# Kernel tuning notes

Hardware: AMD Instinct MI355X
Metric: run time of the kernel (lower is better)

## Reference

```python
import jax, jax.numpy as jnp
import numpy as np

D_MODEL = 1024
N_HEADS = 16
D_K = D_MODEL // N_HEADS
D_FF = 4096
EPS = 1e-6


def setup_inputs() -> dict:
    key = jax.random.key(0)
    ks = jax.random.split(key, 8)
    s = 0.02
    return {
        "x": jax.random.normal(ks[0], (2, 2048, D_MODEL), dtype=jnp.float32),
        "Wq": jax.random.normal(ks[1], (D_MODEL, D_MODEL), dtype=jnp.float32) * s,
        "bq": jnp.zeros((D_MODEL,), jnp.float32),
        "Wk": jax.random.normal(ks[2], (D_MODEL, D_MODEL), dtype=jnp.float32) * s,
        "bk": jnp.zeros((D_MODEL,), jnp.float32),
        "Wv": jax.random.normal(ks[3], (D_MODEL, D_MODEL), dtype=jnp.float32) * s,
        "bv": jnp.zeros((D_MODEL,), jnp.float32),
        "Wo": jax.random.normal(ks[4], (D_MODEL, D_MODEL), dtype=jnp.float32) * s,
        "bo": jnp.zeros((D_MODEL,), jnp.float32),
        "W1": jax.random.normal(ks[5], (D_FF, D_MODEL), dtype=jnp.float32) * s,
        "b1": jnp.zeros((D_FF,), jnp.float32),
        "W2": jax.random.normal(ks[6], (D_MODEL, D_FF), dtype=jnp.float32) * s,
        "b2": jnp.zeros((D_MODEL,), jnp.float32),
        "g1": jnp.ones((D_MODEL,), jnp.float32),
        "be1": jnp.zeros((D_MODEL,), jnp.float32),
        "g2": jnp.ones((D_MODEL,), jnp.float32),
        "be2": jnp.zeros((D_MODEL,), jnp.float32),
    }


def _layernorm(x, gamma, beta):
    mean = x.mean(axis=-1, keepdims=True)
    var = ((x - mean) ** 2).mean(axis=-1, keepdims=True)
    return gamma * (x - mean) / jnp.sqrt(var + EPS) + beta


def _linear(x, W, b):
    # torch nn.Linear: y = x @ W.T + b
    return x @ W.T + b


def reference(x, Wq, bq, Wk, bk, Wv, bv, Wo, bo, W1, b1, W2, b2, g1, be1, g2, be2):
    B, S, _ = x.shape
    h = _layernorm(x, g1, be1)
    # project and split heads -> [B, H, S, d_k]
    Q = _linear(h, Wq, bq).reshape(B, S, N_HEADS, D_K).transpose(0, 2, 1, 3)
    K = _linear(h, Wk, bk).reshape(B, S, N_HEADS, D_K).transpose(0, 2, 1, 3)
    V = _linear(h, Wv, bv).reshape(B, S, N_HEADS, D_K).transpose(0, 2, 1, 3)
    scores = jnp.einsum("bhqd,bhkd->bhqk", Q, K) / jnp.sqrt(jnp.float32(D_K))
    attn = jax.nn.softmax(scores, axis=-1)
    ctx = jnp.einsum("bhqk,bhkd->bhqd", attn, V)
    ctx = ctx.transpose(0, 2, 1, 3).reshape(B, S, D_MODEL)
    x = x + _linear(ctx, Wo, bo)
    h2 = _layernorm(x, g2, be2)
    ff = _linear(jax.nn.gelu(_linear(h2, W1, b1), approximate=False), W2, b2)
    return x + ff
```

## Files before the change

### kernel.cpp

```cpp
#include <hip/hip_runtime.h>
#include <stdint.h>

#define D_MODEL 1024
#define N_HEADS 16
#define DKH     64
#define D_FF    4096
#define BATCH   2
#define SEQ     2048
#define M_TOK   (BATCH*SEQ)

typedef unsigned short u16;
typedef __attribute__((ext_vector_type(8))) short short8;
typedef __attribute__((ext_vector_type(4))) float f32x4;

__device__ __forceinline__ u16 f2b(float f){
  union { float f; uint32_t i; } c; c.f = f;
  uint32_t x = c.i;
  uint32_t r = x + 0x7fffu + ((x >> 16) & 1u);
  return (u16)(r >> 16);
}

__device__ __forceinline__ uint32_t pk_bf16(float a, float b){
  uint32_t d;
  asm("v_cvt_pk_bf16_f32 %0, %1, %2" : "=v"(d) : "v"(a), "v"(b));
  return d;
}

__device__ __forceinline__ void gl_lds16(const u16* g, u16* l){
  __builtin_amdgcn_global_load_lds(
      (const __attribute__((address_space(1))) void*)g,
      (__attribute__((address_space(3))) void*)l, 16, 0, 0);
}

#define MFMA16(a,b,c) __builtin_amdgcn_mfma_f32_16x16x32_bf16((a),(b),(c),0,0,0)

__global__ __launch_bounds__(256) void cvt_ln_kernel(
    const float* __restrict__ s0, const float* __restrict__ s1,
    const float* __restrict__ s2, const float* __restrict__ s3,
    const float* __restrict__ s4, const float* __restrict__ s5,
    u16* __restrict__ d0, u16* __restrict__ d1, u16* __restrict__ d2,
    u16* __restrict__ d3, u16* __restrict__ d4, u16* __restrict__ d5,
    const float* __restrict__ X, const float* __restrict__ G,
    const float* __restrict__ Bt, u16* __restrict__ O)
{
  __shared__ float psum[4], psum2[4];
  if (blockIdx.y == 6){
    const int row = blockIdx.x;
    const int t = threadIdx.x;
    float4 xv = *(const float4*)&X[(size_t)row * D_MODEL + t * 4];
    float s  = xv.x + xv.y + xv.z + xv.w;
    float s2 = xv.x*xv.x + xv.y*xv.y + xv.z*xv.z + xv.w*xv.w;
    #pragma unroll
    for (int off = 32; off >= 1; off >>= 1){
      s  += __shfl_down(s,  off, 64);
      s2 += __shfl_down(s2, off, 64);
    }
    const int wv = t >> 6, ln = t & 63;
    if (ln == 0){ psum[wv] = s; psum2[wv] = s2; }
    __syncthreads();
    float ts  = psum[0] + psum[1] + psum[2] + psum[3];
    float ts2 = psum2[0] + psum2[1] + psum2[2] + psum2[3];
    float mean = ts * (1.f / D_MODEL);
    float var  = ts2 * (1.f / D_MODEL) - mean * mean;
    float rstd = rsqrtf(var + 1e-6f);
    float4 g4 = *(const float4*)&G[t * 4];
    float4 b4 = *(const float4*)&Bt[t * 4];
    ushort4 o;
    o.x = f2b(g4.x * (xv.x - mean) * rstd + b4.x);
    o.y = f2b(g4.y * (xv.y - mean) * rstd + b4.y);
    o.z = f2b(g4.z * (xv.z - mean) * rstd + b4.z);
    o.w = f2b(g4.w * (xv.w - mean) * rstd + b4.w);
    *(ushort4*)&O[(size_t)row * D_MODEL + t * 4] = o;
    return;
  }
  const float* s; u16* d; int n;
  switch (blockIdx.y){
    case 0: s=s0; d=d0; n=D_MODEL*D_MODEL; break;
    case 1: s=s1; d=d1; n=D_MODEL*D_MODEL; break;
    case 2: s=s2; d=d2; n=D_MODEL*D_MODEL; break;
    case 3: s=s3; d=d3; n=D_MODEL*D_MODEL; break;
    case 4: s=s4; d=d4; n=D_FF*D_MODEL;   break;
    default: s=s5; d=d5; n=D_MODEL*D_FF;  break;
  }
  int i = (blockIdx.x * 256 + threadIdx.x) * 4;
  if (i < n){
    float4 f = *(const float4*)&s[i];
    ushort4 o; o.x = f2b(f.x); o.y = f2b(f.y); o.z = f2b(f.z); o.w = f2b(f.w);
    *(ushort4*)&d[i] = o;
  }
}

__global__ __launch_bounds__(256) void ln_kernel(
    const float* __restrict__ X, const float* __restrict__ G,
    const float* __restrict__ Bt, u16* __restrict__ O)
{
  const int row = blockIdx.x;
  const int t = threadIdx.x;
  float4 xv = *(const float4*)&X[(size_t)row * D_MODEL + t * 4];
  float s  = xv.x + xv.y + xv.z + xv.w;
  float s2 = xv.x*xv.x + xv.y*xv.y + xv.z*xv.z + xv.w*xv.w;
  #pragma unroll
  for (int off = 32; off >= 1; off >>= 1){
    s  += __shfl_down(s,  off, 64);
    s2 += __shfl_down(s2, off, 64);
  }
  __shared__ float psum[4], psum2[4];
  const int wv = t >> 6, ln = t & 63;
  if (ln == 0){ psum[wv] = s; psum2[wv] = s2; }
  __syncthreads();
  float ts  = psum[0] + psum[1] + psum[2] + psum[3];
  float ts2 = psum2[0] + psum2[1] + psum2[2] + psum2[3];
  float mean = ts * (1.f / D_MODEL);
  float var  = ts2 * (1.f / D_MODEL) - mean * mean;
  float rstd = rsqrtf(var + 1e-6f);
  float4 g4 = *(const float4*)&G[t * 4];
  float4 b4 = *(const float4*)&Bt[t * 4];
  ushort4 o;
  o.x = f2b(g4.x * (xv.x - mean) * rstd + b4.x);
  o.y = f2b(g4.y * (xv.y - mean) * rstd + b4.y);
  o.z = f2b(g4.z * (xv.z - mean) * rstd + b4.z);
  o.w = f2b(g4.w * (xv.w - mean) * rstd + b4.w);
  *(ushort4*)&O[(size_t)row * D_MODEL + t * 4] = o;
}

template<int EPI, int OUTF, int TM, int BK>
__global__ __launch_bounds__(256,2) void gemm_bt(
    const u16* __restrict__ A, const u16* __restrict__ W,
    const float* __restrict__ bias, const float* resid,
    void* Cout, int K, int Ndim)
{
  constexpr int MI = TM / 32;
  __shared__ __align__(16) u16 sA[TM*BK];
  __shared__ __align__(16) u16 sB[128*BK];
  const int t = threadIdx.x;
  const int w = t >> 6, lane = t & 63, lr = lane & 15, quad = lane >> 4;
  const int wm = (w & 1) * (TM/2), wn = (w >> 1) * 64;
  const int m0 = blockIdx.x * TM, n0 = blockIdx.y * 128;

  f32x4 acc[MI][4];
  #pragma unroll
  for (int i = 0; i < MI; i++)
    #pragma unroll
    for (int j = 0; j < 4; j++) acc[i][j] = (f32x4){0.f,0.f,0.f,0.f};

  for (int k0 = 0; k0 < K; k0 += BK){
    __syncthreads();
    if constexpr (BK == 64){
      const int srow = lane >> 3;
      const int scol = ((lane & 7) ^ srow) * 8;
      #pragma unroll
      for (int it = 0; it < TM/32; it++)
        gl_lds16(&A[(size_t)(m0 + it*32 + w*8 + srow) * K + k0 + scol], &sA[(it*32 + w*8) * 64]);
      #pragma unroll
      for (int it = 0; it < 4; it++)
        gl_lds16(&W[(size_t)(n0 + it*32 + w*8 + srow) * K + k0 + scol], &sB[(it*32 + w*8) * 64]);
    } else {
      const int lro = lane >> 4;
      const int cl  = lane & 15;
      #pragma unroll
      for (int it = 0; it < TM/16; it++){
        int R = w*(TM/4) + it*4;
        int gr = R + lro;
        int gc = (cl ^ (gr & 7)) * 8;
        gl_lds16(&A[(size_t)(m0 + gr) * K + k0 + gc], &sA[R * BK]);
      }
      #pragma unroll
      for (int it = 0; it < 8; it++){
        int R = w*32 + it*4;
        int gr = R + lro;
        int gc = (cl ^ (gr & 7)) * 8;
        gl_lds16(&W[(size_t)(n0 + gr) * K + k0 + gc], &sB[R * BK]);
      }
    }
    __syncthreads();
    #pragma unroll
    for (int ks = 0; ks < BK/32; ks++){
      short8 af[MI], bfr[4];
      #pragma unroll
      for (int i = 0; i < MI; i++)
        af[i]  = *(const short8*)&sA[(wm + i*16 + lr)*BK + (((ks*4 + quad) ^ (lr & 7)) * 8)];
      #pragma unroll
      for (int j = 0; j < 4; j++)
        bfr[j] = *(const short8*)&sB[(wn + j*16 + lr)*BK + (((ks*4 + quad) ^ (lr & 7)) * 8)];
      #pragma unroll
      for (int i = 0; i < MI; i++)
        #pragma unroll
        for (int j = 0; j < 4; j++)
          acc[i][j] = MFMA16(af[i], bfr[j], acc[i][j]);
    }
  }

  #pragma unroll
  for (int j = 0; j < 4; j++){
    int gn = n0 + wn + j*16 + lr;
    float bb = bias[gn];
    #pragma unroll
    for (int i = 0; i < MI; i++){
      #pragma unroll
      for (int r = 0; r < 4; r++){
        int gm = m0 + wm + i*16 + quad*4 + r;
        size_t idx = (size_t)gm * Ndim + gn;
        float v = acc[i][j][r] + bb;
        if (EPI == 1){
          float p = v * (1.59576912f + 0.07135481f * v * v);
          float e = __builtin_amdgcn_exp2f(-1.44269504f * p);
          v = v * __builtin_amdgcn_rcpf(1.f + e);
        }
        if (EPI == 2) v += resid[idx];
        if (OUTF) ((float*)Cout)[idx] = v;
        else      ((u16*)Cout)[idx] = f2b(v);
      }
    }
  }
}

__global__ __launch_bounds__(256,2) void gemm_qkv(
    const u16* __restrict__ A,
    const u16* __restrict__ Wq, const float* __restrict__ bq,
    const u16* __restrict__ Wk, const float* __restrict__ bk,
    const u16* __restrict__ Wv, const float* __restrict__ bv,
    u16* __restrict__ Qo, u16* __restrict__ Ko, u16* __restrict__ Vo)
{
  __shared__ __align__(16) u16 sA[128*64];
  __shared__ __align__(16) u16 sB[128*64];
  const u16* W; const float* bias; u16* out; float scale;
  if (blockIdx.z == 0){ W = Wq; bias = bq; out = Qo; scale = 0.125f * 1.44269504f; }
  else if (blockIdx.z == 1){ W = Wk; bias = bk; out = Ko; scale = 1.f; }
  else { W = Wv; bias = bv; out = Vo; scale = 1.f; }

  const int t = threadIdx.x;
  const int w = t >> 6, lane = t & 63, lr = lane & 15, quad = lane >> 4;
  const int wm = (w & 1) * 64, wn = (w >> 1) * 64;
  const int m0 = blockIdx.x * 128, n0 = blockIdx.y * 128;
  const int srow = lane >> 3;
  const int scol = ((lane & 7) ^ srow) * 8;
  const int K = D_MODEL;

  f32x4 acc[4][4];
  #pragma unroll
  for (int i = 0; i < 4; i++)
    #pragma unroll
    for (int j = 0; j < 4; j++) acc[i][j] = (f32x4){0.f,0.f,0.f,0.f};

  for (int k0 = 0; k0 < K; k0 += 64){
    __syncthreads();
    #pragma unroll
    for (int it = 0; it < 4; it++){
      gl_lds16(&A[(size_t)(m0 + it*32 + w*8 + srow) * K + k0 + scol], &sA[(it*32 + w*8) * 64]);
      gl_lds16(&W[(size_t)(n0 + it*32 + w*8 + srow) * K + k0 + scol], &sB[(it*32 + w*8) * 64]);
    }
    __syncthreads();
    #pragma unroll
    for (int ks = 0; ks < 2; ks++){
      short8 af[4], bfr[4];
      #pragma unroll
      for (int i = 0; i < 4; i++)
        af[i]  = *(const short8*)&sA[(wm + i*16 + lr)*64 + (((ks*4 + quad) ^ (lr & 7)) * 8)];
      #pragma unroll
      for (int j = 0; j < 4; j++)
        bfr[j] = *(const short8*)&sB[(wn + j*16 + lr)*64 + (((ks*4 + quad) ^ (lr & 7)) * 8)];
      #pragma unroll
      for (int i = 0; i < 4; i++)
        #pragma unroll
        for (int j = 0; j < 4; j++)
          acc[i][j] = MFMA16(af[i], bfr[j], acc[i][j]);
    }
  }

  #pragma unroll
  for (int j = 0; j < 4; j++){
    int gn = n0 + wn + j*16 + lr;
    int hh = gn >> 6, d = gn & 63;
    float bb = bias[gn];
    #pragma unroll
    for (int i = 0; i < 4; i++){
      #pragma unroll
      for (int r = 0; r < 4; r++){
        int gm = m0 + wm + i*16 + quad*4 + r;
        int b = gm >> 11, sq = gm & 2047;
        float v = (acc[i][j][r] + bb) * scale;
        out[(((size_t)(b * N_HEADS + hh)) * SEQ + sq) * DKH + d] = f2b(v);
      }
    }
  }
}

__global__ __launch_bounds__(256) void transpose_v(
    const u16* __restrict__ V, u16* __restrict__ Vt)
{
  __shared__ __align__(16) u16 st[64][72];
  const int s0 = blockIdx.x * 64, bh = blockIdx.y, t = threadIdx.x;
  const u16* vp = V + (size_t)bh * SEQ * DKH;
  u16* op = Vt + (size_t)bh * DKH * SEQ;
  #pragma unroll
  for (int it = 0; it < 2; it++){
    int c = it * 256 + t, r = c >> 3, cc = c & 7;
    *(float4*)&st[r][cc*8] = *(const float4*)&vp[(size_t)(s0 + r) * DKH + cc*8];
  }
  __syncthreads();
  #pragma unroll
  for (int it = 0; it < 2; it++){
    int c = it * 256 + t, d = c >> 3, sc = c & 7;
    u16 tmp[8];
    #pragma unroll
    for (int e = 0; e < 8; e++) tmp[e] = st[sc*8 + e][d];
    float4 f; __builtin_memcpy(&f, tmp, 16);
    *(float4*)&op[(size_t)d * SEQ + s0 + sc*8] = f;
  }
}

__global__ __launch_bounds__(256,2) void attn_kernel(
    const u16* __restrict__ Q, const u16* __restrict__ K,
    const u16* __restrict__ Vt, u16* __restrict__ ctx)
{
  __shared__ __align__(16) u16 sK[128][72];
  __shared__ __align__(16) u16 sVt[64][136];
  __shared__ __align__(16) u16 sP[4][32][136];

  const int t = threadIdx.x, w = t >> 6, lane = t & 63;
  const int lr = lane & 15, quad = lane >> 4;
  const int bh = blockIdx.x;
  const int q0 = blockIdx.y * 128;
  const u16* Qp = Q + ((size_t)bh * SEQ + q0) * DKH;
  const u16* Kp = K + (size_t)bh * SEQ * DKH;
  const u16* Vp = Vt + (size_t)bh * DKH * SEQ;

  short8 qf[2][2];
  #pragma unroll
  for (int i = 0; i < 2; i++)
    #pragma unroll
    for (int ks = 0; ks < 2; ks++)
      qf[i][ks] = *(const short8*)&Qp[(size_t)(w*32 + i*16 + lr) * DKH + ks*32 + quad*8];

  short8 ones;
  #pragma unroll
  for (int e = 0; e < 8; e++) ones[e] = (short)0x3F80;

  f32x4 acco[2][4];
  f32x4 accl[2];
  #pragma unroll
  for (int i = 0; i < 2; i++){
    accl[i] = (f32x4){0.f,0.f,0.f,0.f};
    #pragma unroll
    for (int jc = 0; jc < 4; jc++) acco[i][jc] = (f32x4){0.f,0.f,0.f,0.f};
  }

  for (int kt = 0; kt < SEQ/128; kt++){
    const int s0 = kt * 128;
    __syncthreads();
    #pragma unroll
    for (int it = 0; it < 4; it++){
      int c = it * 256 + t, r = c >> 3, cc = c & 7;
      *(float4*)&sK[r][cc*8] = *(const float4*)&Kp[(size_t)(s0 + r) * DKH + cc*8];
    }
    #pragma unroll
    for (int it = 0; it < 4; it++){
      int c = it * 256 + t, d = c >> 4, sc = c & 15;
      *(float4*)&sVt[d][sc*8] = *(const float4*)&Vp[(size_t)d * SEQ + s0 + sc*8];
    }
    __syncthreads();

    f32x4 st_[2][8];
    #pragma unroll
    for (int i = 0; i < 2; i++)
      #pragma unroll
      for (int j = 0; j < 8; j++) st_[i][j] = (f32x4){0.f,0.f,0.f,0.f};
    #pragma unroll
    for (int ks = 0; ks < 2; ks++){
      #pragma unroll
      for (int j = 0; j < 8; j++){
        short8 kf = *(const short8*)&sK[j*16 + lr][ks*32 + quad*8];
        st_[0][j] = MFMA16(kf, qf[0][ks], st_[0][j]);
        st_[1][j] = MFMA16(kf, qf[1][ks], st_[1][j]);
      }
    }

    #pragma unroll
    for (int i = 0; i < 2; i++)
      #pragma unroll
      for (int j = 0; j < 8; j++){
        float p0 = __builtin_amdgcn_exp2f(st_[i][j][0]);
        float p1 = __builtin_amdgcn_exp2f(st_[i][j][1]);
        float p2 = __builtin_amdgcn_exp2f(st_[i][j][2]);
        float p3 = __builtin_amdgcn_exp2f(st_[i][j][3]);
        uint2 pv; pv.x = pk_bf16(p0, p1); pv.y = pk_bf16(p2, p3);
        *(uint2*)&sP[w][i*16 + lr][j*16 + quad*4] = pv;
      }

    #pragma unroll
    for (int ks = 0; ks < 4; ks++){
      short8 pf0 = *(const short8*)&sP[w][lr     ][ks*32 + quad*8];
      short8 pf1 = *(const short8*)&sP[w][16 + lr][ks*32 + quad*8];
      accl[0] = MFMA16(pf0, ones, accl[0]);
      accl[1] = MFMA16(pf1, ones, accl[1]);
      #pragma unroll
      for (int jc = 0; jc < 4; jc++){
        short8 vf = *(const short8*)&sVt[jc*16 + lr][ks*32 + quad*8];
        acco[0][jc] = MFMA16(pf0, vf, acco[0][jc]);
        acco[1][jc] = MFMA16(pf1, vf, acco[1][jc]);
      }
    }
  }

  const int bq = bh >> 4, hh = bh & 15;
  u16* op = ctx + ((size_t)bq * SEQ + q0) * D_MODEL + hh * DKH;
  #pragma unroll
  for (int i = 0; i < 2; i++){
    #pragma unroll
    for (int r = 0; r < 4; r++){
      float rl = 1.f / accl[i][r];
      int row = w*32 + i*16 + quad*4 + r;
      #pragma unroll
      for (int jc = 0; jc < 4; jc++)
        op[(size_t)row * D_MODEL + jc*16 + lr] = f2b(acco[i][jc][r] * rl);
    }
  }
}

extern "C" void kernel_launch(void* const* d_in, const int* in_sizes, int n_in,
                              void* d_out, int out_size, void* d_ws, size_t ws_size,
                              hipStream_t stream)
{
  const float* x   = (const float*)d_in[0];
  const float* Wq  = (const float*)d_in[1];
  const float* bq  = (const float*)d_in[2];
  const float* Wk  = (const float*)d_in[3];
  const float* bk  = (const float*)d_in[4];
  const float* Wv  = (const float*)d_in[5];
  const float* bv  = (const float*)d_in[6];
  const float* Wo  = (const float*)d_in[7];
  const float* bo  = (const float*)d_in[8];
  const float* W1  = (const float*)d_in[9];
  const float* b1  = (const float*)d_in[10];
  const float* W2  = (const float*)d_in[11];
  const float* b2  = (const float*)d_in[12];
  const float* g1  = (const float*)d_in[13];
  const float* be1 = (const float*)d_in[14];
  const float* g2  = (const float*)d_in[15];
  const float* be2 = (const float*)d_in[16];

  char* ws = (char*)d_ws;
  const size_t MB = 1024ull * 1024ull;
  u16* wqb = (u16*)(ws + 0*MB);
  u16* wkb = (u16*)(ws + 2*MB);
  u16* wvb = (u16*)(ws + 4*MB);
  u16* wob = (u16*)(ws + 6*MB);
  u16* w1b = (u16*)(ws + 8*MB);
  u16* w2b = (u16*)(ws + 16*MB);
  u16* h   = (u16*)(ws + 24*MB);
  u16* q   = (u16*)(ws + 32*MB);
  u16* k   = (u16*)(ws + 40*MB);
  u16* v   = (u16*)(ws + 48*MB);
  u16* vt  = (u16*)(ws + 56*MB);
  u16* ff  = (u16*)(ws + 32*MB);
  u16* ctx = v;
  u16* h2  = h;
  float* x1 = (float*)d_out;

  cvt_ln_kernel<<<dim3(4096, 7), 256, 0, stream>>>(
      Wq, Wk, Wv, Wo, W1, W2, wqb, wkb, wvb, wob, w1b, w2b,
      x, g1, be1, h);

  gemm_qkv<<<dim3(M_TOK/128, D_MODEL/128, 3), 256, 0, stream>>>(
      h, wqb, bq, wkb, bk, wvb, bv, q, k, v);
  transpose_v<<<dim3(SEQ/64, BATCH*N_HEADS), 256, 0, stream>>>(v, vt);
  attn_kernel<<<dim3(BATCH*N_HEADS, SEQ/128), 256, 0, stream>>>(q, k, vt, ctx);
  gemm_bt<2,1,64,128><<<dim3(M_TOK/64, D_MODEL/128), 256, 0, stream>>>(
      ctx, wob, bo, x, (void*)x1, D_MODEL, D_MODEL);
  ln_kernel<<<M_TOK, 256, 0, stream>>>(x1, g2, be2, h2);
  gemm_bt<1,0,128,64><<<dim3(M_TOK/128, D_FF/128), 256, 0, stream>>>(
      h2, w1b, b1, nullptr, (void*)ff, D_MODEL, D_FF);
  gemm_bt<2,1,64,128><<<dim3(M_TOK/64, D_MODEL/128), 256, 0, stream>>>(
      ff, w2b, b2, x1, d_out, D_FF, D_MODEL);
}
```

Before: 347.7 us.

## Fuse V transpose into QKV GEMM epilogue and rework attention with async LDS loads

The V projection epilogue now stages its tile in shared memory and writes V already transposed to [bh][d][seq], so the separate transpose_v kernel and its extra global round trip go away. The attention kernel moves to 512 threads, with each wave owning 16 query rows instead of 32. K and V tiles are loaded with direct global-to-LDS copies (gl_lds16) into XOR-swizzled unpadded layouts, and the P buffer is swizzled the same way. The smaller per-wave work cuts register pressure and raises the number of waves per block, at the cost of more waves sharing each K/V tile and barrier.

```diff
diff --git a/kernel.cpp b/kernel.cpp
--- a/kernel.cpp
+++ b/kernel.cpp
@@ -221,12 +221,13 @@
     const u16* __restrict__ Wv, const float* __restrict__ bv,
     u16* __restrict__ Qo, u16* __restrict__ Ko, u16* __restrict__ Vo)
 {
-  __shared__ __align__(16) u16 sA[128*64];
-  __shared__ __align__(16) u16 sB[128*64];
-  const u16* W; const float* bias; u16* out; float scale;
-  if (blockIdx.z == 0){ W = Wq; bias = bq; out = Qo; scale = 0.125f * 1.44269504f; }
-  else if (blockIdx.z == 1){ W = Wk; bias = bk; out = Ko; scale = 1.f; }
-  else { W = Wv; bias = bv; out = Vo; scale = 1.f; }
+  __shared__ __align__(16) u16 smem[2*128*64];
+  u16* sA = smem;
+  u16* sB = smem + 128*64;
+  const u16* W; const float* bias; float scale;
+  if (blockIdx.z == 0){ W = Wq; bias = bq; scale = 0.125f * 1.44269504f; }
+  else if (blockIdx.z == 1){ W = Wk; bias = bk; scale = 1.f; }
+  else { W = Wv; bias = bv; scale = 1.f; }
 
   const int t = threadIdx.x;
   const int w = t >> 6, lane = t & 63, lr = lane & 15, quad = lane >> 4;
@@ -267,6 +268,36 @@
     }
   }
 
+  if (blockIdx.z == 2){
+    __syncthreads();
+    #pragma unroll
+    for (int j = 0; j < 4; j++){
+      int dl = wn + j*16 + lr;
+      float bb = bias[n0 + dl];
+      #pragma unroll
+      for (int i = 0; i < 4; i++){
+        #pragma unroll
+        for (int r = 0; r < 4; r++){
+          int tok = wm + i*16 + quad*4 + r;
+          int phys = (((tok >> 3) ^ (dl & 7)) * 8) + (tok & 7);
+          smem[dl*128 + phys] = f2b(acc[i][j][r] + bb);
+        }
+      }
+    }
+    __syncthreads();
+    const int b = m0 >> 11, sq0 = m0 & 2047, hh0 = n0 >> 6;
+    #pragma unroll
+    for (int it = 0; it < 8; it++){
+      int idx = it*256 + t;
+      int drow = idx >> 4, c = idx & 15;
+      float4 val = *(const float4*)&smem[drow*128 + ((c ^ (drow & 7)) * 8)];
+      int hh = hh0 + (drow >> 6), d = drow & 63;
+      *(float4*)&Vo[(((size_t)(b*N_HEADS + hh))*DKH + d)*SEQ + sq0 + c*8] = val;
+    }
+    return;
+  }
+
+  u16* out = (blockIdx.z == 0) ? Qo : Ko;
   #pragma unroll
   for (int j = 0; j < 4; j++){
     int gn = n0 + wn + j*16 + lr;
@@ -285,37 +316,13 @@
   }
 }
 
-__global__ __launch_bounds__(256) void transpose_v(
-    const u16* __restrict__ V, u16* __restrict__ Vt)
-{
-  __shared__ __align__(16) u16 st[64][72];
-  const int s0 = blockIdx.x * 64, bh = blockIdx.y, t = threadIdx.x;
-  const u16* vp = V + (size_t)bh * SEQ * DKH;
-  u16* op = Vt + (size_t)bh * DKH * SEQ;
-  #pragma unroll
-  for (int it = 0; it < 2; it++){
-    int c = it * 256 + t, r = c >> 3, cc = c & 7;
-    *(float4*)&st[r][cc*8] = *(const float4*)&vp[(size_t)(s0 + r) * DKH + cc*8];
-  }
-  __syncthreads();
-  #pragma unroll
-  for (int it = 0; it < 2; it++){
-    int c = it * 256 + t, d = c >> 3, sc = c & 7;
-    u16 tmp[8];
-    #pragma unroll
-    for (int e = 0; e < 8; e++) tmp[e] = st[sc*8 + e][d];
-    float4 f; __builtin_memcpy(&f, tmp, 16);
-    *(float4*)&op[(size_t)d * SEQ + s0 + sc*8] = f;
-  }
-}
-
-__global__ __launch_bounds__(256,2) void attn_kernel(
+__global__ __launch_bounds__(512,2) void attn_kernel(
     const u16* __restrict__ Q, const u16* __restrict__ K,
     const u16* __restrict__ Vt, u16* __restrict__ ctx)
 {
-  __shared__ __align__(16) u16 sK[128][72];
-  __shared__ __align__(16) u16 sVt[64][136];
-  __shared__ __align__(16) u16 sP[4][32][136];
+  __shared__ __align__(16) u16 sK[128*64];
+  __shared__ __align__(16) u16 sVt[64*128];
+  __shared__ __align__(16) u16 sP[8*16*128];
 
   const int t = threadIdx.x, w = t >> 6, lane = t & 63;
   const int lr = lane & 15, quad = lane >> 4;
@@ -325,79 +332,72 @@
   const u16* Kp = K + (size_t)bh * SEQ * DKH;
   const u16* Vp = Vt + (size_t)bh * DKH * SEQ;
 
-  short8 qf[2][2];
-  #pragma unroll
-  for (int i = 0; i < 2; i++)
-    #pragma unroll
-    for (int ks = 0; ks < 2; ks++)
-      qf[i][ks] = *(const short8*)&Qp[(size_t)(w*32 + i*16 + lr) * DKH + ks*32 + quad*8];
+  short8 qf[2];
+  #pragma unroll
+  for (int ks = 0; ks < 2; ks++)
+    qf[ks] = *(const short8*)&Qp[(size_t)(w*16 + lr) * DKH + ks*32 + quad*8];
 
   short8 ones;
   #pragma unroll
   for (int e = 0; e < 8; e++) ones[e] = (short)0x3F80;
 
-  f32x4 acco[2][4];
-  f32x4 accl[2];
-  #pragma unroll
-  for (int i = 0; i < 2; i++){
-    accl[i] = (f32x4){0.f,0.f,0.f,0.f};
-    #pragma unroll
-    for (int jc = 0; jc < 4; jc++) acco[i][jc] = (f32x4){0.f,0.f,0.f,0.f};
-  }
+  f32x4 acco[4];
+  f32x4 accl;
+  accl = (f32x4){0.f,0.f,0.f,0.f};
+  #pragma unroll
+  for (int jc = 0; jc < 4; jc++) acco[jc] = (f32x4){0.f,0.f,0.f,0.f};
+
+  const int srow = lane >> 3;
+  const int sc8  = ((lane & 7) ^ srow) * 8;
+  const int lro  = lane >> 4, cl = lane & 15;
 
   for (int kt = 0; kt < SEQ/128; kt++){
     const int s0 = kt * 128;
     __syncthreads();
     #pragma unroll
-    for (int it = 0; it < 4; it++){
-      int c = it * 256 + t, r = c >> 3, cc = c & 7;
-      *(float4*)&sK[r][cc*8] = *(const float4*)&Kp[(size_t)(s0 + r) * DKH + cc*8];
-    }
-    #pragma unroll
-    for (int it = 0; it < 4; it++){
-      int c = it * 256 + t, d = c >> 4, sc = c & 15;
-      *(float4*)&sVt[d][sc*8] = *(const float4*)&Vp[(size_t)d * SEQ + s0 + sc*8];
-    }
-    __syncthreads();
-
-    f32x4 st_[2][8];
-    #pragma unroll
-    for (int i = 0; i < 2; i++)
-      #pragma unroll
-      for (int j = 0; j < 8; j++) st_[i][j] = (f32x4){0.f,0.f,0.f,0.f};
+    for (int it = 0; it < 2; it++)
+      gl_lds16(&Kp[(size_t)(s0 + it*64 + w*8 + srow) * DKH + sc8],
+               &sK[(it*64 + w*8) * 64]);
+    #pragma unroll
+    for (int it = 0; it < 2; it++){
+      int R = w*8 + it*4;
+      int gr = R + lro;
+      int gc = (cl ^ (gr & 7)) * 8;
+      gl_lds16(&Vp[(size_t)gr * SEQ + s0 + gc], &sVt[R * 128]);
+    }
+    __syncthreads();
+
+    f32x4 st_[8];
+    #pragma unroll
+    for (int j = 0; j < 8; j++) st_[j] = (f32x4){0.f,0.f,0.f,0.f};
     #pragma unroll
     for (int ks = 0; ks < 2; ks++){
       #pragma unroll
       for (int j = 0; j < 8; j++){
-        short8 kf = *(const short8*)&sK[j*16 + lr][ks*32 + quad*8];
-        st_[0][j] = MFMA16(kf, qf[0][ks], st_[0][j]);
-        st_[1][j] = MFMA16(kf, qf[1][ks], st_[1][j]);
-      }
-    }
-
-    #pragma unroll
-    for (int i = 0; i < 2; i++)
-      #pragma unroll
-      for (int j = 0; j < 8; j++){
-        float p0 = __builtin_amdgcn_exp2f(st_[i][j][0]);
-        float p1 = __builtin_amdgcn_exp2f(st_[i][j][1]);
-        float p2 = __builtin_amdgcn_exp2f(st_[i][j][2]);
-        float p3 = __builtin_amdgcn_exp2f(st_[i][j][3]);
-        uint2 pv; pv.x = pk_bf16(p0, p1); pv.y = pk_bf16(p2, p3);
-        *(uint2*)&sP[w][i*16 + lr][j*16 + quad*4] = pv;
-      }
+        short8 kf = *(const short8*)&sK[(j*16 + lr)*64 + (((ks*4 + quad) ^ (lr & 7)) * 8)];
+        st_[j] = MFMA16(kf, qf[ks], st_[j]);
+      }
+    }
+
+    #pragma unroll
+    for (int j = 0; j < 8; j++){
+      float p0 = __builtin_amdgcn_exp2f(st_[j][0]);
+      float p1 = __builtin_amdgcn_exp2f(st_[j][1]);
+      float p2 = __builtin_amdgcn_exp2f(st_[j][2]);
+      float p3 = __builtin_amdgcn_exp2f(st_[j][3]);
+      uint2 pv; pv.x = pk_bf16(p0, p1); pv.y = pk_bf16(p2, p3);
+      int c = j*2 + (quad >> 1);
+      *(uint2*)&sP[w*2048 + lr*128 + ((c ^ (lr & 7)) * 8) + (quad & 1)*4] = pv;
+    }
 
     #pragma unroll
     for (int ks = 0; ks < 4; ks++){
-      short8 pf0 = *(const short8*)&sP[w][lr     ][ks*32 + quad*8];
-      short8 pf1 = *(const short8*)&sP[w][16 + lr][ks*32 + quad*8];
-      accl[0] = MFMA16(pf0, ones, accl[0]);
-      accl[1] = MFMA16(pf1, ones, accl[1]);
+      short8 pf = *(const short8*)&sP[w*2048 + lr*128 + (((ks*4 + quad) ^ (lr & 7)) * 8)];
+      accl = MFMA16(pf, ones, accl);
       #pragma unroll
       for (int jc = 0; jc < 4; jc++){
-        short8 vf = *(const short8*)&sVt[jc*16 + lr][ks*32 + quad*8];
-        acco[0][jc] = MFMA16(pf0, vf, acco[0][jc]);
-        acco[1][jc] = MFMA16(pf1, vf, acco[1][jc]);
+        short8 vf = *(const short8*)&sVt[(jc*16 + lr)*128 + (((ks*4 + quad) ^ (lr & 7)) * 8)];
+        acco[jc] = MFMA16(pf, vf, acco[jc]);
       }
     }
   }
@@ -405,15 +405,12 @@
   const int bq = bh >> 4, hh = bh & 15;
   u16* op = ctx + ((size_t)bq * SEQ + q0) * D_MODEL + hh * DKH;
   #pragma unroll
-  for (int i = 0; i < 2; i++){
-    #pragma unroll
-    for (int r = 0; r < 4; r++){
-      float rl = 1.f / accl[i][r];
-      int row = w*32 + i*16 + quad*4 + r;
-      #pragma unroll
-      for (int jc = 0; jc < 4; jc++)
-        op[(size_t)row * D_MODEL + jc*16 + lr] = f2b(acco[i][jc][r] * rl);
-    }
+  for (int r = 0; r < 4; r++){
+    float rl = 1.f / accl[r];
+    int row = w*16 + quad*4 + r;
+    #pragma unroll
+    for (int jc = 0; jc < 4; jc++)
+      op[(size_t)row * D_MODEL + jc*16 + lr] = f2b(acco[jc][r] * rl);
   }
 }
 
@@ -450,10 +447,9 @@
   u16* h   = (u16*)(ws + 24*MB);
   u16* q   = (u16*)(ws + 32*MB);
   u16* k   = (u16*)(ws + 40*MB);
-  u16* v   = (u16*)(ws + 48*MB);
+  u16* ctx = (u16*)(ws + 48*MB);
   u16* vt  = (u16*)(ws + 56*MB);
   u16* ff  = (u16*)(ws + 32*MB);
-  u16* ctx = v;
   u16* h2  = h;
   float* x1 = (float*)d_out;
 
@@ -462,9 +458,8 @@
       x, g1, be1, h);
 
   gemm_qkv<<<dim3(M_TOK/128, D_MODEL/128, 3), 256, 0, stream>>>(
-      h, wqb, bq, wkb, bk, wvb, bv, q, k, v);
-  transpose_v<<<dim3(SEQ/64, BATCH*N_HEADS), 256, 0, stream>>>(v, vt);
-  attn_kernel<<<dim3(BATCH*N_HEADS, SEQ/128), 256, 0, stream>>>(q, k, vt, ctx);
+      h, wqb, bq, wkb, bk, wvb, bv, q, k, vt);
+  attn_kernel<<<dim3(BATCH*N_HEADS, SEQ/128), 512, 0, stream>>>(q, k, vt, ctx);
   gemm_bt<2,1,64,128><<<dim3(M_TOK/64, D_MODEL/128), 256, 0, stream>>>(
       ctx, wob, bo, x, (void*)x1, D_MODEL, D_MODEL);
   ln_kernel<<<M_TOK, 256, 0, stream>>>(x1, g2, be2, h2);
```

Result: faster. 325.4 us (-6.4%).
